# Performance work log

Measured on AMD Instinct MI355X. Metric: run time of the kernel, lower is better.

## Reference

```python
import jax, jax.numpy as jnp
import numpy as np

B, N, DE, DH, L, DC = 8, 256, 768, 192, 2, 192
NEG = 1e30  # mask_logic constant from the repo


def setup_inputs() -> dict:
    ks = iter(jax.random.split(jax.random.key(0), 32))

    def nrm(shape, s=0.02):
        return jax.random.normal(next(ks), shape, dtype=jnp.float32) * s

    features = jax.random.normal(next(ks), (B, N, DE), dtype=jnp.float32)
    # DAG adjacency: node i attends to a subset of j < i; guarantee edge (i, i-1)
    rnd = jax.random.bernoulli(next(ks), 0.3, (B, N, N))
    tril = jnp.tril(jnp.ones((N, N), jnp.bool_), -1)
    adj = ((rnd & tril[None]) | jnp.eye(N, k=-1, dtype=jnp.bool_)[None]).astype(jnp.float32)
    s_mask = jax.random.bernoulli(next(ks), 0.5, (B, N, N)).astype(jnp.float32)
    s_mask_onehot = jnp.stack([1.0 - s_mask, s_mask], axis=-1)  # unused in forward
    lengths = jnp.full((B,), N, dtype=jnp.int32)  # unused (nodal_att_type=None)
    return dict(
        features=features, adj=adj, s_mask=s_mask,
        s_mask_onehot=s_mask_onehot, lengths=lengths,
        fc1_w=nrm((DE, DH)), fc1_b=jnp.zeros((DH,), jnp.float32),
        gat_w=nrm((L, 2 * DH)), gat_b=jnp.zeros((L,), jnp.float32),
        wr0=nrm((L, DH, DH)), wr1=nrm((L, DH, DH)),
        gruc_wih=nrm((L, 3 * DH, DH)), gruc_whh=nrm((L, 3 * DH, DH)),
        gruc_bih=jnp.zeros((L, 3 * DH), jnp.float32),
        gruc_bhh=jnp.zeros((L, 3 * DH), jnp.float32),
        grup_wih=nrm((L, 3 * DH, DH)), grup_whh=nrm((L, 3 * DH, DH)),
        grup_bih=jnp.zeros((L, 3 * DH), jnp.float32),
        grup_bhh=jnp.zeros((L, 3 * DH), jnp.float32),
        mlp_w0=nrm((DH * (L + 1), DH)), mlp_b0=jnp.zeros((DH,), jnp.float32),
        mlp_w1=nrm((DH, DH)), mlp_b1=jnp.zeros((DH,), jnp.float32),
        mlp_w2=nrm((DH, DC)), mlp_b2=jnp.zeros((DC,), jnp.float32),
    )


def _gru(x, h, wih, whh, bih, bhh):
    # torch.nn.GRUCell math
    gi = x @ wih.T + bih
    gh = h @ whh.T + bhh
    ir, iz, inn = jnp.split(gi, 3, axis=-1)
    hr, hz, hn = jnp.split(gh, 3, axis=-1)
    r = jax.nn.sigmoid(ir + hr)
    z = jax.nn.sigmoid(iz + hz)
    n = jnp.tanh(inn + r * hn)
    return (1.0 - z) * n + z * h


def _layer(Hl, adj, s_mask, gat_w, gat_b, wr0, wr1, cw, cp):
    # One DAG layer: sequential scan over nodes. Carry holds the relation-
    # projected value buffers V0=H1@Wr0^T, V1=H1@Wr1^T and per-node key
    # scores Ksc=H1@wk (rows >= i are zero and masked out), which is
    # mathematically identical to the torch code that re-projects the
    # growing H1 every step.
    wq, wk = gat_w[:DH], gat_w[DH:]
    pos = jnp.arange(N)

    def step(carry, xs):
        V0, V1, Ksc = carry
        i, x_i, adj_i, sm_i = xs  # x_i:(B,DH) adj_i,sm_i:(B,N)
        score = (x_i @ wq)[:, None] + Ksc + gat_b          # (B,N)
        mask = (pos < i)[None, :] & (adj_i > 0.5)          # ragged :i slice
        alpha = jnp.where(mask, score, score - NEG)        # mask_logic
        attn = jax.nn.softmax(alpha, axis=-1)              # masked -> exactly 0
        Vrel = V0 * sm_i[..., None] + V1 * (1.0 - sm_i[..., None])
        M = jnp.einsum('bn,bnd->bd', attn, Vrel)
        M = jnp.where(i > 0, M, 0.0)                       # node 0: no context
        C = _gru(x_i, M, *cw)
        P = _gru(M, x_i, *cp)
        Hnew = C + P
        V0 = V0.at[:, i, :].set(Hnew @ wr0.T)
        V1 = V1.at[:, i, :].set(Hnew @ wr1.T)
        Ksc = Ksc.at[:, i].set(Hnew @ wk)
        attn_out = jnp.where(i > 0, attn, 0.0)             # adjB row 0 is zeros
        return (V0, V1, Ksc), (Hnew, attn_out)

    z3 = jnp.zeros((B, N, DH), jnp.float32)
    carry0 = (z3, z3, jnp.zeros((B, N), jnp.float32))
    xs = (pos, Hl.transpose(1, 0, 2), adj.transpose(1, 0, 2), s_mask.transpose(1, 0, 2))
    _, (Hseq, Aseq) = jax.lax.scan(step, carry0, xs)
    return Hseq.transpose(1, 0, 2), Aseq.transpose(1, 0, 2)  # (B,N,DH),(B,N,N)


def reference(features, adj, s_mask, s_mask_onehot, lengths,
              fc1_w, fc1_b, gat_w, gat_b, wr0, wr1,
              gruc_wih, gruc_whh, gruc_bih, gruc_bhh,
              grup_wih, grup_whh, grup_bih, grup_bhh,
              mlp_w0, mlp_b0, mlp_w1, mlp_b1, mlp_w2, mlp_b2):
    Hl = jax.nn.relu(features @ fc1_w + fc1_b)  # H0
    Hs, As = [Hl], []
    for l in range(L):
        cw = (gruc_wih[l], gruc_whh[l], gruc_bih[l], gruc_bhh[l])
        cp = (grup_wih[l], grup_whh[l], grup_bih[l], grup_bhh[l])
        Hl, Al = _layer(Hl, adj, s_mask, gat_w[l], gat_b[l], wr0[l], wr1[l], cw, cp)
        Hs.append(Hl)
        As.append(Al)
    H = jnp.concatenate(Hs, axis=2)  # (B,N,DH*(L+1))
    # nodal_att_type=None => attentive_node_features is identity
    h = jax.nn.relu(H @ mlp_w0 + mlp_b0)
    h = jax.nn.relu(h @ mlp_w1 + mlp_b1)  # mlp_layers-1 = 1 extra block
    logits = h @ mlp_w2 + mlp_b2          # dropout: eval-mode identity
    return logits, jnp.stack(As, axis=1)  # (B,N,DC), (B,L,N,N)
```

## Files before the change

kernel.cpp:

```cpp
#include <hip/hip_runtime.h>
#include <stdint.h>

#define B_  8
#define N_  256
#define DH_ 192
#define L_  2
#define G3  576
#define G6  1152
#define NW  4
#define DS  48
#define KD  24
#define GC  288
#define STH 10001
#define STP 20001
#define STQ 25001
#define SPK 50000
#define SF1 50001
#define SF2 50002
#define SDN 60001

typedef unsigned long long u64;

__device__ __forceinline__ float bflo(uint32_t u) { return __uint_as_float(u << 16); }
__device__ __forceinline__ float bfhi(uint32_t u) { return __uint_as_float(u & 0xffff0000u); }
__device__ __forceinline__ uint32_t f2bf(float f) {
    uint32_t x = __float_as_uint(f);
    x += 0x7fffu + ((x >> 16) & 1u);
    return x >> 16;
}
__device__ __forceinline__ float sigm(float x)  { return 1.f / (1.f + __expf(-x)); }
__device__ __forceinline__ float tanhf_(float x){ return 1.f - 2.f / (1.f + __expf(2.f * x)); }
__device__ __forceinline__ u64 packvs(float v, int st) {
    return ((u64)(uint32_t)st << 32) | __float_as_uint(v);
}
__device__ __forceinline__ u64 agload(const u64* p) {
    return __hip_atomic_load(p, __ATOMIC_RELAXED, __HIP_MEMORY_SCOPE_AGENT);
}
__device__ __forceinline__ void agstore(u64* p, u64 v) {
    __hip_atomic_store(p, v, __ATOMIC_RELAXED, __HIP_MEMORY_SCOPE_AGENT);
}

struct ScanSm {
    uint4 Wr4s[12 * DH_];
    float sA0[2][N_], sA1[2][N_], sKsc[N_];
    float sAdjN[N_], sSmN[N_];
    float sXq[DH_], sPre[6 * DS], sXv[DS];
    float sM[DH_], su0[DS], su1[DS], sGc[GC], sHn[DS];
    float sRedS[2][4], sRedX[3], sSaved[4];
};
struct WorkSm {
    float sX[DH_];
    float sPv[GC];
    float sRed[3];
};
struct PrologSm {
    float sA[8][768];
    float sRed[3][8][192];
};
struct MlpSm {
    float sH[8][576];
    float sRed[3][8][192];
    float sT[8][192];
};
union SmemAll { ScanSm s; WorkSm w; PrologSm p; MlpSm m; };

__device__ void prepack_slice(int idx,
    const float* __restrict__ wr0, const float* __restrict__ wr1,
    const float* __restrict__ c_wih, const float* __restrict__ c_whh,
    const float* __restrict__ c_bih, const float* __restrict__ c_bhh,
    const float* __restrict__ p_wih, const float* __restrict__ p_whh,
    const float* __restrict__ p_bih, const float* __restrict__ p_bhh,
    float* __restrict__ WpreT, uint32_t* __restrict__ W4,
    uint32_t* __restrict__ Wr4, uint32_t* __restrict__ Wp4w,
    float* __restrict__ biasPre, float* __restrict__ gbx)
{
    for (int l = 0; l < L_; ++l) {
        const float* cwih = c_wih + l * G3 * DH_;
        const float* cwhh = c_whh + l * G3 * DH_;
        const float* pwih = p_wih + l * G3 * DH_;
        const float* pwhh = p_whh + l * G3 * DH_;
        if (l == 0) {
            int k = idx / G6, r = idx - k * G6;
            float w = (r < G3) ? cwih[r * DH_ + k] : pwhh[(r - G3) * DH_ + k];
            WpreT[k * G6 + r] = w;
        }
        if (idx < NW * 27648) {
            int w = idx / 27648, pos = idx % 27648;
            int p4 = pos / 1152, rem = pos % 1152;
            int c2 = rem >> 2, s = rem & 3;
            int p = 4 * p4 + s;
            int j = c2 / DS, dd = c2 % DS;
            int c = 192 * j + DS * w + dd;
            float w0 = (c < G3) ? cwhh[c * DH_ + 2 * p]     : pwih[(c - G3) * DH_ + 2 * p];
            float w1 = (c < G3) ? cwhh[c * DH_ + 2 * p + 1] : pwih[(c - G3) * DH_ + 2 * p + 1];
            W4[l * NW * 27648 + idx] = f2bf(w0) | (f2bf(w1) << 16);
            if (l == 1) {
                int r = c;
                float v0 = (r < G3) ? cwih[r * DH_ + 2 * p]     : pwhh[(r - G3) * DH_ + 2 * p];
                float v1 = (r < G3) ? cwih[r * DH_ + 2 * p + 1] : pwhh[(r - G3) * DH_ + 2 * p + 1];
                Wp4w[idx] = f2bf(v0) | (f2bf(v1) << 16);
            }
        }
        if (idx < NW * 9216) {
            int w = idx / 9216, pos = idx % 9216;
            int kq = pos / 768, rem = pos % 768;
            int d = rem >> 2, s = rem & 3;
            int k = DS * w + 4 * kq + s;
            Wr4[l * NW * 9216 + idx] =
                f2bf(wr0[l * DH_ * DH_ + d * DH_ + k]) |
                (f2bf(wr1[l * DH_ * DH_ + d * DH_ + k]) << 16);
        }
        if (idx < G6) {
            float base = (idx < G3) ? c_bih[l * G3 + idx] : p_bhh[l * G3 + idx - G3];
            float fold = 0.f;
            if (idx < 384)                    fold = c_bhh[l * G3 + idx];
            else if (idx >= G3 && idx < 960)  fold = p_bih[l * G3 + idx - G3];
            biasPre[l * G6 + idx] = base + fold;
        }
        if (idx < 384) {
            gbx[l * 384 + idx] = (idx < DH_) ? c_bhh[l * G3 + 384 + idx]
                                             : p_bih[l * G3 + 384 + (idx - DH_)];
        }
    }
}

__device__ void flag_sync(u64* flags, int wgid, int t, int stamp)
{
    __threadfence();
    __syncthreads();
    if (t == 0) agstore(&flags[wgid], packvs(0.f, stamp));
    if (t < 96) {
        while ((uint32_t)(agload(&flags[t]) >> 32) != (uint32_t)stamp) {}
    }
    __syncthreads();
    __threadfence();
    __syncthreads();
}

__device__ void prologue(char* smem, int wgid, int t,
    const float* __restrict__ features, const float* __restrict__ fc1_w,
    const float* __restrict__ fc1_b, const float* __restrict__ WpreT,
    const float* __restrict__ biasPre,
    float* __restrict__ Hcat, float* __restrict__ PREg, u64* __restrict__ Fp)
{
    PrologSm* P = (PrologSm*)smem;
    const int c = t % 192, kg = t / 192;
    for (int tt = wgid; tt < 256; tt += 96) {
        const int r0 = tt * 8;
        for (int q = t; q < 1536; q += 576) {
            int r = q / 192, c4 = q % 192;
            *(float4*)&P->sA[r][4 * c4] = *(const float4*)(features + (size_t)(r0 + r) * 768 + 4 * c4);
        }
        __syncthreads();
        {
            const float* bp = fc1_w + (size_t)(kg * 256) * 192 + c;
            float acc[8] = {0.f, 0.f, 0.f, 0.f, 0.f, 0.f, 0.f, 0.f};
            #pragma unroll 8
            for (int kk = 0; kk < 256; ++kk) {
                float bv = bp[(size_t)kk * 192];
                #pragma unroll
                for (int rr = 0; rr < 8; ++rr) acc[rr] += P->sA[rr][kg * 256 + kk] * bv;
            }
            #pragma unroll
            for (int rr = 0; rr < 8; ++rr) P->sRed[kg][rr][c] = acc[rr];
        }
        __syncthreads();
        if (t < 192) {
            float bv = fc1_b[t];
            #pragma unroll
            for (int rr = 0; rr < 8; ++rr) {
                float v = P->sRed[0][rr][t] + P->sRed[1][rr][t] + P->sRed[2][rr][t] + bv;
                Hcat[(size_t)(r0 + rr) * G3 + t] = fmaxf(v, 0.f);
            }
        }
        __syncthreads();
    }
    flag_sync(Fp + 96, wgid, t, SF1);
    {
        const float bpa = biasPre[t], bpb = biasPre[576 + t];
        for (int tt = wgid; tt < 256; tt += 96) {
            const int r0 = tt * 8;
            for (int q = t; q < 384; q += 576) {
                int r = q / 48, c4 = q % 48;
                *(float4*)&P->sA[r][4 * c4] = *(const float4*)(Hcat + (size_t)(r0 + r) * G3 + 4 * c4);
            }
            __syncthreads();
            {
                const float* b0 = WpreT + t;
                float a0[8] = {0.f,0.f,0.f,0.f,0.f,0.f,0.f,0.f};
                float a1[8] = {0.f,0.f,0.f,0.f,0.f,0.f,0.f,0.f};
                #pragma unroll 4
                for (int k = 0; k < 192; ++k) {
                    float bva = b0[(size_t)k * G6];
                    float bvb = b0[(size_t)k * G6 + 576];
                    #pragma unroll
                    for (int rr = 0; rr < 8; ++rr) {
                        float av = P->sA[rr][k];
                        a0[rr] += av * bva; a1[rr] += av * bvb;
                    }
                }
                #pragma unroll
                for (int rr = 0; rr < 8; ++rr) {
                    PREg[(size_t)(r0 + rr) * G6 + t]       = a0[rr] + bpa;
                    PREg[(size_t)(r0 + rr) * G6 + 576 + t] = a1[rr] + bpb;
                }
            }
            __syncthreads();
        }
    }
    flag_sync(Fp + 192, wgid, t, SF2);
}

__device__ void mlp_tail(char* smem, int wgid, int t,
    const float* __restrict__ Hcat,
    const float* __restrict__ mw0, const float* __restrict__ mb0,
    const float* __restrict__ mw1, const float* __restrict__ mb1,
    const float* __restrict__ mw2, const float* __restrict__ mb2,
    float* __restrict__ out, u64* __restrict__ Fd)
{
    if (t < 64) {
        while ((uint32_t)(agload(&Fd[t]) >> 32) != (uint32_t)SDN) {}
    }
    __syncthreads();
    __threadfence();
    __syncthreads();
    MlpSm* M = (MlpSm*)smem;
    const int c = t % 192, kg = t / 192;
    for (int tt = wgid; tt < 256; tt += 96) {
        const int r0 = tt * 8;
        for (int q = t; q < 1152; q += 576) {
            int r = q / 144, c4 = q % 144;
            *(float4*)&M->sH[r][4 * c4] = *(const float4*)(Hcat + (size_t)(r0 + r) * G3 + 4 * c4);
        }
        __syncthreads();
        {
            const float* bp = mw0 + (size_t)(kg * 192) * 192 + c;
            float acc[8] = {0.f,0.f,0.f,0.f,0.f,0.f,0.f,0.f};
            #pragma unroll 8
            for (int kk = 0; kk < 192; ++kk) {
                float bv = bp[(size_t)kk * 192];
                #pragma unroll
                for (int rr = 0; rr < 8; ++rr) acc[rr] += M->sH[rr][kg * 192 + kk] * bv;
            }
            #pragma unroll
            for (int rr = 0; rr < 8; ++rr) M->sRed[kg][rr][c] = acc[rr];
        }
        __syncthreads();
        if (t < 192) {
            float bv = mb0[t];
            #pragma unroll
            for (int rr = 0; rr < 8; ++rr)
                M->sT[rr][t] = fmaxf(M->sRed[0][rr][t] + M->sRed[1][rr][t] + M->sRed[2][rr][t] + bv, 0.f);
        }
        __syncthreads();
        {
            const float* bp = mw1 + (size_t)(kg * 64) * 192 + c;
            float acc[8] = {0.f,0.f,0.f,0.f,0.f,0.f,0.f,0.f};
            #pragma unroll 8
            for (int kk = 0; kk < 64; ++kk) {
                float bv = bp[(size_t)kk * 192];
                #pragma unroll
                for (int rr = 0; rr < 8; ++rr) acc[rr] += M->sT[rr][kg * 64 + kk] * bv;
            }
            #pragma unroll
            for (int rr = 0; rr < 8; ++rr) M->sRed[kg][rr][c] = acc[rr];
        }
        __syncthreads();
        if (t < 192) {
            float bv = mb1[t];
            #pragma unroll
            for (int rr = 0; rr < 8; ++rr)
                M->sH[rr][t] = fmaxf(M->sRed[0][rr][t] + M->sRed[1][rr][t] + M->sRed[2][rr][t] + bv, 0.f);
        }
        __syncthreads();
        {
            const float* bp = mw2 + (size_t)(kg * 64) * 192 + c;
            float acc[8] = {0.f,0.f,0.f,0.f,0.f,0.f,0.f,0.f};
            #pragma unroll 8
            for (int kk = 0; kk < 64; ++kk) {
                float bv = bp[(size_t)kk * 192];
                #pragma unroll
                for (int rr = 0; rr < 8; ++rr) acc[rr] += M->sH[rr][kg * 64 + kk] * bv;
            }
            #pragma unroll
            for (int rr = 0; rr < 8; ++rr) M->sRed[kg][rr][c] = acc[rr];
        }
        __syncthreads();
        if (t < 192) {
            float bv = mb2[t];
            #pragma unroll
            for (int rr = 0; rr < 8; ++rr)
                out[(size_t)(r0 + rr) * 192 + t] =
                    M->sRed[0][rr][t] + M->sRed[1][rr][t] + M->sRed[2][rr][t] + bv;
        }
        __syncthreads();
    }
}

template<int ISL2>
__device__ void scan_body(
    ScanSm* S, int b, int w, int t,
    const float* __restrict__ xin, float* __restrict__ hout,
    const float* __restrict__ PREg, const float* __restrict__ adj,
    const float* __restrict__ smask,
    const uint32_t* __restrict__ W4l, const uint32_t* __restrict__ Wr4l,
    const float* __restrict__ gbxl, const float* __restrict__ gatwl,
    uint32_t* __restrict__ Hw, u64* __restrict__ MPsl, u64* __restrict__ Kdl,
    u64* __restrict__ HcW, const u64* __restrict__ HcR,
    const u64* __restrict__ PREcR, const u64* __restrict__ XQcR,
    float* __restrict__ AsB, int sbase)
{
    const int lane = t & 63, wave = t >> 6;
    const int dg0 = w * DS;
    const float* adjB = adj   + (size_t)b * N_ * N_;
    const float* smB  = smask + (size_t)b * N_ * N_;
    const int fi = b * NW;
    const int cB4 = t >> 1, khB4 = t & 1;

    {
        uint32_t* wr = (uint32_t*)S->Wr4s;
        for (int q = t; q < 9216; q += 576) wr[q] = Wr4l[q];
    }
    uint4 wreg[12];
    {
        const uint4* W4v = (const uint4*)W4l;
        #pragma unroll
        for (int p4 = 0; p4 < 12; ++p4) wreg[p4] = W4v[(12 * khB4 + p4) * GC + cB4];
    }
    float wqv = (!ISL2 && t < DH_) ? gatwl[t] : 0.f;
    float wkv = 0.f, g2b = 0.f, g5b = 0.f;
    if (t < DS) { wkv = gatwl[DH_ + dg0 + t]; g2b = gbxl[dg0 + t]; g5b = gbxl[DH_ + dg0 + t]; }
    if (t < N_) { S->sKsc[t] = 0.f; S->sA0[1][t] = 0.f; S->sA1[1][t] = 0.f; }
    if (t < DS) { S->su0[t] = 0.f; S->su1[t] = 0.f; }
    if (t < 4)  S->sRedS[1][t] = 0.f;
    if (w == 0 && t < N_) AsB[t] = 0.f;

    if (!ISL2) {
        if (t < DS) {
            const float* pre = PREg + (size_t)(b * N_) * G6 + dg0 + t;
            S->sPre[t] = pre[0]; S->sPre[DS + t] = pre[192]; S->sPre[2 * DS + t] = pre[384];
            S->sPre[3 * DS + t] = pre[576]; S->sPre[4 * DS + t] = pre[768]; S->sPre[5 * DS + t] = pre[960];
            S->sXv[t] = xin[(size_t)(b * N_) * G3 + dg0 + t];
        }
        for (int q = t; q < 176; q += 576) {
            if (q < 64)       *(float4*)&S->sAdjN[4 * q] = *(const float4*)(adjB + N_ + 4 * q);
            else if (q < 128) { int q2 = q - 64;  *(float4*)&S->sSmN[4 * q2] = *(const float4*)(smB + N_ + 4 * q2); }
            else              { int q2 = q - 128; *(float4*)&S->sXq[4 * q2] = *(const float4*)(xin + (size_t)(b * N_ + 1) * G3 + 4 * q2); }
        }
    } else {
        for (int q = t; q < 321; q += 576) {
            if (q < 64)       *(float4*)&S->sAdjN[4 * q] = *(const float4*)(adjB + N_ + 4 * q);
            else if (q < 128) { int q2 = q - 64;  *(float4*)&S->sSmN[4 * q2] = *(const float4*)(smB + N_ + 4 * q2); }
            else if (q < 176) {
                int d = q - 128;
                const u64* p = HcR + ((size_t)(b * N_) * NW + w) * DS + d;
                u64 v; do { v = agload(p); } while ((uint32_t)(v >> 32) != (uint32_t)STH);
                S->sXv[d] = __uint_as_float((uint32_t)v);
            } else if (q < 320) {
                int qq = q - 176;
                const u64* p = PREcR + ((size_t)(b * N_) * NW + w) * 144 + qq;
                u64 v; do { v = agload(p); } while ((uint32_t)(v >> 32) != (uint32_t)STP);
                uint32_t pl = (uint32_t)v;
                S->sPre[2 * qq] = bflo(pl); S->sPre[2 * qq + 1] = bfhi(pl);
            } else {
                const u64* p = XQcR + b * N_ + 1;
                u64 v; do { v = agload(p); } while ((uint32_t)(v >> 32) != (uint32_t)(STQ + 1));
                S->sSaved[3] = __uint_as_float((uint32_t)v);
            }
        }
    }
    __syncthreads();
    {
        float hn = 0.f;
        if (t < DS) {
            float xv = S->sXv[t];
            float r1 = sigm(S->sPre[t]), z1 = sigm(S->sPre[DS + t]);
            float n1 = tanhf_(S->sPre[2 * DS + t] + r1 * g2b);
            float Cv = (1.f - z1) * n1;
            float r2 = sigm(S->sPre[3 * DS + t]), z2 = sigm(S->sPre[4 * DS + t]);
            float n2 = tanhf_(g5b + r2 * S->sPre[5 * DS + t]);
            hn = Cv + (1.f - z2) * n2 + z2 * xv;
            S->sHn[t] = hn;
            hout[(size_t)(b * N_) * G3 + dg0 + t] = hn;
            if (!ISL2) HcW[((size_t)(b * N_) * NW + w) * DS + t] = packvs(hn, STH);
        }
        if (t == 0) { S->sSaved[0] = S->sAdjN[0]; S->sSaved[1] = S->sSmN[0]; }
        if (wave == 0) {
            float v = hn * wkv;
            #pragma unroll
            for (int o = 32; o; o >>= 1) v += __shfl_xor(v, o);
            if (lane == 0) agstore(&Kdl[fi + w], packvs(v, sbase));
        }
    }
    __syncthreads();
    if (t < KD) Hw[(size_t)t * N_] = f2bf(S->sHn[2 * t]) | (f2bf(S->sHn[2 * t + 1]) << 16);
    if (!ISL2) {
        float px = (t < DH_) ? S->sXq[t] * wqv : 0.f;
        #pragma unroll
        for (int o = 32; o; o >>= 1) px += __shfl_xor(px, o);
        if (t < DH_ && lane == 0) S->sRedX[wave] = px;
    }
    __syncthreads();
    float xqc = ISL2 ? S->sSaved[3] : (S->sRedX[0] + S->sRedX[1] + S->sRedX[2]);

    for (int i = 1; i < N_; ++i) {
        const int row = b * N_ + i;
        const int stamp = sbase + i;
        const int pp = i & 1, pn = pp ^ 1;

        if (t >= 384) {
            const int u = t - 384;
            const int inx = (i + 1 < N_) ? i + 1 : N_ - 1;
            if (!ISL2) {
                for (int qq = u; qq < 260; qq += 192) {
                    if (qq < 64)
                        *(float4*)&S->sAdjN[4 * qq] = *(const float4*)(adjB + (size_t)inx * N_ + 4 * qq);
                    else if (qq < 128) { int q2 = qq - 64;
                        *(float4*)&S->sSmN[4 * q2] = *(const float4*)(smB + (size_t)inx * N_ + 4 * q2); }
                    else if (qq < 140) { int q2 = qq - 128;
                        *(float4*)&S->sXv[4 * q2] = *(const float4*)(xin + (size_t)row * G3 + dg0 + 4 * q2); }
                    else if (qq < 212) { int q2 = qq - 140; int g = q2 / 12, o = q2 - 12 * g;
                        *(float4*)&S->sPre[g * DS + 4 * o] =
                            *(const float4*)(PREg + (size_t)row * G6 + g * DH_ + dg0 + 4 * o); }
                    else { int q2 = qq - 212;
                        *(float4*)&S->sXq[4 * q2] = *(const float4*)(xin + (size_t)(b * N_ + inx) * G3 + 4 * q2); }
                }
            } else {
                for (int qq = u; qq < 321; qq += 192) {
                    if (qq < 64)
                        *(float4*)&S->sAdjN[4 * qq] = *(const float4*)(adjB + (size_t)inx * N_ + 4 * qq);
                    else if (qq < 128) { int q2 = qq - 64;
                        *(float4*)&S->sSmN[4 * q2] = *(const float4*)(smB + (size_t)inx * N_ + 4 * q2); }
                    else if (qq < 176) {
                        int d = qq - 128;
                        const u64* p = HcR + ((size_t)row * NW + w) * DS + d;
                        u64 v; do { v = agload(p); } while ((uint32_t)(v >> 32) != (uint32_t)(STH + i));
                        S->sXv[d] = __uint_as_float((uint32_t)v);
                    } else if (qq < 320) {
                        int q2 = qq - 176;
                        const u64* p = PREcR + ((size_t)row * NW + w) * 144 + q2;
                        u64 v; do { v = agload(p); } while ((uint32_t)(v >> 32) != (uint32_t)(STP + i));
                        uint32_t pl = (uint32_t)v;
                        S->sPre[2 * q2] = bflo(pl); S->sPre[2 * q2 + 1] = bfhi(pl);
                    } else {
                        const u64* p = XQcR + b * N_ + inx;
                        u64 v; do { v = agload(p); } while ((uint32_t)(v >> 32) != (uint32_t)(STQ + inx));
                        S->sSaved[3] = __uint_as_float((uint32_t)v);
                    }
                }
            }
            if (t == 575) {
                const uint32_t ex = (uint32_t)(stamp - 1);
                u64 k0, k1, k2, k3;
                do {
                    k0 = agload(&Kdl[fi + 0]); k1 = agload(&Kdl[fi + 1]);
                    k2 = agload(&Kdl[fi + 2]); k3 = agload(&Kdl[fi + 3]);
                } while ((uint32_t)(k0 >> 32) != ex || (uint32_t)(k1 >> 32) != ex ||
                         (uint32_t)(k2 >> 32) != ex || (uint32_t)(k3 >> 32) != ex);
                float kdot = __uint_as_float((uint32_t)k0) + __uint_as_float((uint32_t)k1)
                           + __uint_as_float((uint32_t)k2) + __uint_as_float((uint32_t)k3);
                float adjI1 = S->sSaved[0], smI1 = S->sSaved[1];
                float e1 = (adjI1 > 0.5f) ? __expf(xqc + kdot) : 0.f;
                float Ssum = S->sRedS[pp][0] + S->sRedS[pp][1] + S->sRedS[pp][2] + S->sRedS[pp][3] + e1;
                S->sKsc[i - 1] = kdot;
                float c0 = e1 * smI1;
                S->sA0[pp][i - 1] = c0; S->sA1[pp][i - 1] = e1 - c0;
                S->sSaved[2] = 1.f / Ssum;
            }
        }
        __syncthreads();

        if (t < DH_) {
            float mp = 0.f, h0a = 0.f, h1a = 0.f;
            #pragma unroll 4
            for (int kq = 0; kq < 12; ++kq) {
                uint4 wv = S->Wr4s[kq * DH_ + t];
                const int k0 = 4 * kq;
                float lo, hi;
                lo = bflo(wv.x); hi = bfhi(wv.x);
                mp = fmaf(S->su0[k0 + 0], lo, mp); mp = fmaf(S->su1[k0 + 0], hi, mp);
                h0a = fmaf(S->sHn[k0 + 0], lo, h0a); h1a = fmaf(S->sHn[k0 + 0], hi, h1a);
                lo = bflo(wv.y); hi = bfhi(wv.y);
                mp = fmaf(S->su0[k0 + 1], lo, mp); mp = fmaf(S->su1[k0 + 1], hi, mp);
                h0a = fmaf(S->sHn[k0 + 1], lo, h0a); h1a = fmaf(S->sHn[k0 + 1], hi, h1a);
                lo = bflo(wv.z); hi = bfhi(wv.z);
                mp = fmaf(S->su0[k0 + 2], lo, mp); mp = fmaf(S->su1[k0 + 2], hi, mp);
                h0a = fmaf(S->sHn[k0 + 2], lo, h0a); h1a = fmaf(S->sHn[k0 + 2], hi, h1a);
                lo = bflo(wv.w); hi = bfhi(wv.w);
                mp = fmaf(S->su0[k0 + 3], lo, mp); mp = fmaf(S->su1[k0 + 3], hi, mp);
                h0a = fmaf(S->sHn[k0 + 3], lo, h0a); h1a = fmaf(S->sHn[k0 + 3], hi, h1a);
            }
            float invS = S->sSaved[2];
            mp = (mp + S->sA0[pp][i - 1] * h0a + S->sA1[pp][i - 1] * h1a) * invS;
            S->sM[t] = mp;
            agstore(&MPsl[(size_t)(fi + w) * DH_ + t], packvs(mp, stamp));
            if (!ISL2) {
                float px = S->sXq[t] * wqv;
                #pragma unroll
                for (int o = 32; o; o >>= 1) px += __shfl_xor(px, o);
                if (lane == 0) S->sRedX[wave] = px;
            }
        } else if (w == 0 && t < 448) {
            int j = t - 192;
            AsB[(size_t)i * N_ + j] = (S->sA0[pp][j] + S->sA1[pp][j]) * S->sSaved[2];
        }
        __syncthreads();

        const float xqn = ISL2 ? S->sSaved[3] : (S->sRedX[0] + S->sRedX[1] + S->sRedX[2]);
        if (t < N_) {
            float e = 0.f;
            if (t == i) { S->sSaved[0] = S->sAdjN[t]; S->sSaved[1] = S->sSmN[t]; }
            if (t < i && S->sAdjN[t] > 0.5f) e = __expf(xqn + S->sKsc[t]);
            float b0 = e * S->sSmN[t];
            S->sA0[pn][t] = b0; S->sA1[pn][t] = e - b0;
            float ps = e;
            #pragma unroll
            for (int o = 32; o; o >>= 1) ps += __shfl_xor(ps, o);
            if (lane == 0) S->sRedS[pn][wave] = ps;
        }
        __syncthreads();

        if (t < 384) {
            const int ilim = i;
            const int kd = t >> 4, jp = t & 15;
            const uint32_t* hp = Hw + (size_t)kd * N_;
            float u0l = 0.f, u0h = 0.f, u1l = 0.f, u1h = 0.f;
            int j = jp;
            while (j + 48 < ilim) {
                uint32_t h0 = hp[j], h1 = hp[j + 16], h2 = hp[j + 32], h3 = hp[j + 48];
                float b0, b1;
                b0 = S->sA0[pn][j];      b1 = S->sA1[pn][j];
                u0l = fmaf(b0, bflo(h0), u0l); u0h = fmaf(b0, bfhi(h0), u0h);
                u1l = fmaf(b1, bflo(h0), u1l); u1h = fmaf(b1, bfhi(h0), u1h);
                b0 = S->sA0[pn][j + 16]; b1 = S->sA1[pn][j + 16];
                u0l = fmaf(b0, bflo(h1), u0l); u0h = fmaf(b0, bfhi(h1), u0h);
                u1l = fmaf(b1, bflo(h1), u1l); u1h = fmaf(b1, bfhi(h1), u1h);
                b0 = S->sA0[pn][j + 32]; b1 = S->sA1[pn][j + 32];
                u0l = fmaf(b0, bflo(h2), u0l); u0h = fmaf(b0, bfhi(h2), u0h);
                u1l = fmaf(b1, bflo(h2), u1l); u1h = fmaf(b1, bfhi(h2), u1h);
                b0 = S->sA0[pn][j + 48]; b1 = S->sA1[pn][j + 48];
                u0l = fmaf(b0, bflo(h3), u0l); u0h = fmaf(b0, bfhi(h3), u0h);
                u1l = fmaf(b1, bflo(h3), u1l); u1h = fmaf(b1, bfhi(h3), u1h);
                j += 64;
            }
            for (; j < ilim; j += 16) {
                uint32_t hv = hp[j];
                float b0 = S->sA0[pn][j], b1 = S->sA1[pn][j];
                u0l = fmaf(b0, bflo(hv), u0l); u0h = fmaf(b0, bfhi(hv), u0h);
                u1l = fmaf(b1, bflo(hv), u1l); u1h = fmaf(b1, bfhi(hv), u1h);
            }
            #pragma unroll
            for (int o = 1; o <= 8; o <<= 1) {
                u0l += __shfl_xor(u0l, o); u0h += __shfl_xor(u0h, o);
                u1l += __shfl_xor(u1l, o); u1h += __shfl_xor(u1h, o);
            }
            if (jp == 0) {
                S->su0[2 * kd] = u0l; S->su0[2 * kd + 1] = u0h;
                S->su1[2 * kd] = u1l; S->su1[2 * kd + 1] = u1h;
            }
        } else {
            const int d = t - 384;
            const int w1 = (w + 1) & 3, w2 = (w + 2) & 3, w3 = (w + 3) & 3;
            u64* pA = &MPsl[(size_t)(fi + w1) * DH_ + d];
            u64* pB = &MPsl[(size_t)(fi + w2) * DH_ + d];
            u64* pC = &MPsl[(size_t)(fi + w3) * DH_ + d];
            const uint32_t ex = (uint32_t)stamp;
            u64 vA, vB, vC;
            do {
                vA = agload(pA); vB = agload(pB); vC = agload(pC);
            } while ((uint32_t)(vA >> 32) != ex || (uint32_t)(vB >> 32) != ex ||
                     (uint32_t)(vC >> 32) != ex);
            S->sM[d] += __uint_as_float((uint32_t)vA)
                      + __uint_as_float((uint32_t)vB)
                      + __uint_as_float((uint32_t)vC);
        }
        __syncthreads();

        {
            float g = 0.f;
            #pragma unroll
            for (int p4 = 0; p4 < 12; ++p4) {
                const uint4 wv = wreg[p4];
                const int m0 = 8 * (12 * khB4 + p4);
                g = fmaf(S->sM[m0 + 0], bflo(wv.x), g); g = fmaf(S->sM[m0 + 1], bfhi(wv.x), g);
                g = fmaf(S->sM[m0 + 2], bflo(wv.y), g); g = fmaf(S->sM[m0 + 3], bfhi(wv.y), g);
                g = fmaf(S->sM[m0 + 4], bflo(wv.z), g); g = fmaf(S->sM[m0 + 5], bfhi(wv.z), g);
                g = fmaf(S->sM[m0 + 6], bflo(wv.w), g); g = fmaf(S->sM[m0 + 7], bfhi(wv.w), g);
            }
            g += __shfl_xor(g, 1);
            if (khB4 == 0) S->sGc[cB4] = g;
        }
        __syncthreads();

        {
            float hn = 0.f;
            if (t < DS) {
                float Mv = S->sM[dg0 + t];
                float r1 = sigm(S->sPre[t] + S->sGc[t]);
                float z1 = sigm(S->sPre[DS + t] + S->sGc[DS + t]);
                float n1 = tanhf_(S->sPre[2 * DS + t] + r1 * (S->sGc[2 * DS + t] + g2b));
                float Cv = (1.f - z1) * n1 + z1 * Mv;
                float r2 = sigm(S->sGc[3 * DS + t] + S->sPre[3 * DS + t]);
                float z2 = sigm(S->sGc[4 * DS + t] + S->sPre[4 * DS + t]);
                float n2 = tanhf_(S->sGc[5 * DS + t] + g5b + r2 * S->sPre[5 * DS + t]);
                hn = Cv + (1.f - z2) * n2 + z2 * S->sXv[t];
                S->sHn[t] = hn;
                hout[(size_t)row * G3 + dg0 + t] = hn;
                if (!ISL2) HcW[((size_t)row * NW + w) * DS + t] = packvs(hn, STH + i);
            }
            if (wave == 0) {
                float v = hn * wkv;
                #pragma unroll
                for (int o = 32; o; o >>= 1) v += __shfl_xor(v, o);
                if (lane == 0) agstore(&Kdl[fi + w], packvs(v, stamp));
            }
            if (t < KD) Hw[(size_t)t * N_ + i] = f2bf(S->sHn[2 * t]) | (f2bf(S->sHn[2 * t + 1]) << 16);
        }
        __syncthreads();
        xqc = xqn;
    }
}

__device__ void worker_body(WorkSm* Wm, int b, int w, int t,
    const uint32_t* __restrict__ Wp4g, const float* __restrict__ bias2,
    const float* __restrict__ wq2,
    const u64* __restrict__ HcR, u64* __restrict__ PREcW, u64* __restrict__ XQcW)
{
    const int lane = t & 63, wave = t >> 6;
    const int c = t >> 1, kh = t & 1;
    uint4 wpreg[12];
    {
        const uint4* v4 = (const uint4*)Wp4g;
        #pragma unroll
        for (int p4 = 0; p4 < 12; ++p4) wpreg[p4] = v4[(12 * kh + p4) * GC + c];
    }
    float bv = 0.f;
    if (kh == 0) bv = bias2[192 * (c / DS) + w * DS + (c % DS)];
    float wqt = (t < DH_) ? wq2[t] : 0.f;
    for (int i = 0; i < N_; ++i) {
        if (t < DH_) {
            const u64* p = HcR + ((size_t)(b * N_ + i) * NW + (t / DS)) * DS + (t % DS);
            u64 v; do { v = agload(p); } while ((uint32_t)(v >> 32) != (uint32_t)(STH + i));
            Wm->sX[t] = __uint_as_float((uint32_t)v);
        }
        __syncthreads();
        {
            float g = 0.f;
            #pragma unroll
            for (int p4 = 0; p4 < 12; ++p4) {
                const uint4 wv = wpreg[p4];
                const int m0 = 8 * (12 * kh + p4);
                g = fmaf(Wm->sX[m0 + 0], bflo(wv.x), g); g = fmaf(Wm->sX[m0 + 1], bfhi(wv.x), g);
                g = fmaf(Wm->sX[m0 + 2], bflo(wv.y), g); g = fmaf(Wm->sX[m0 + 3], bfhi(wv.y), g);
                g = fmaf(Wm->sX[m0 + 4], bflo(wv.z), g); g = fmaf(Wm->sX[m0 + 5], bfhi(wv.z), g);
                g = fmaf(Wm->sX[m0 + 6], bflo(wv.w), g); g = fmaf(Wm->sX[m0 + 7], bfhi(wv.w), g);
            }
            g += __shfl_xor(g, 1);
            if (kh == 0) Wm->sPv[c] = g + bv;
        }
        if (w == 0) {
            float px = (t < DH_) ? Wm->sX[t] * wqt : 0.f;
            #pragma unroll
            for (int o = 32; o; o >>= 1) px += __shfl_xor(px, o);
            if (t < DH_ && lane == 0) Wm->sRed[wave] = px;
        }
        __syncthreads();
        if (t < 144) {
            u64 v = ((u64)(uint32_t)(STP + i) << 32)
                  | f2bf(Wm->sPv[2 * t]) | (f2bf(Wm->sPv[2 * t + 1]) << 16);
            agstore(&PREcW[((size_t)(b * N_ + i) * NW + w) * 144 + t], v);
        }
        if (w == 0 && t == 0)
            agstore(&XQcW[b * N_ + i],
                    packvs(Wm->sRed[0] + Wm->sRed[1] + Wm->sRed[2], STQ + i));
        __syncthreads();
    }
}

__global__ __launch_bounds__(576, 1) void pipeline_kernel(
    const float* __restrict__ features, const float* __restrict__ fc1_w,
    const float* __restrict__ fc1_b,
    const float* __restrict__ adj, const float* __restrict__ smask,
    const float* __restrict__ gatw,
    const float* __restrict__ wr0, const float* __restrict__ wr1,
    const float* __restrict__ c_wih, const float* __restrict__ c_whh,
    const float* __restrict__ c_bih, const float* __restrict__ c_bhh,
    const float* __restrict__ p_wih, const float* __restrict__ p_whh,
    const float* __restrict__ p_bih, const float* __restrict__ p_bhh,
    const float* __restrict__ mw0, const float* __restrict__ mb0,
    const float* __restrict__ mw1, const float* __restrict__ mb1,
    const float* __restrict__ mw2, const float* __restrict__ mb2,
    float* __restrict__ Hcat, float* __restrict__ PREg,
    float* __restrict__ WpreT, uint32_t* __restrict__ W4,
    uint32_t* __restrict__ Wr4, uint32_t* __restrict__ Wp4w,
    float* __restrict__ biasPre, float* __restrict__ gbx,
    uint32_t* __restrict__ Hb, u64* __restrict__ MPs, u64* __restrict__ Kd,
    u64* __restrict__ Hc, u64* __restrict__ PREc, u64* __restrict__ XQc,
    u64* __restrict__ Fp, u64* __restrict__ Fd,
    float* __restrict__ out)
{
    __shared__ __align__(16) char smem[sizeof(SmemAll)];
    const int blk = blockIdx.x, t = threadIdx.x;
    const int wgid = blk;
    const int b = blk & 7, r12 = blk >> 3;
    const int role = r12 >> 2, w = r12 & 3;

    for (int j = 0; j < 4; ++j) {
        int idx = wgid * 576 + t + 55296 * j;
        prepack_slice(idx, wr0, wr1, c_wih, c_whh, c_bih, c_bhh,
                      p_wih, p_whh, p_bih, p_bhh,
                      WpreT, W4, Wr4, Wp4w, biasPre, gbx);
    }
    flag_sync(Fp, wgid, t, SPK);

    prologue(smem, wgid, t, features, fc1_w, fc1_b, WpreT, biasPre,
             Hcat, PREg, Fp);

    float* As = out + 393216;
    if (role == 0) {
        scan_body<0>((ScanSm*)smem, b, w, t,
            Hcat, Hcat + 192, PREg, adj, smask,
            W4, Wr4, gbx, gatw,
            Hb + (size_t)(b * NW + w) * KD * N_, MPs, Kd,
            Hc, nullptr, nullptr, nullptr,
            As + (size_t)b * (L_ * N_ * N_), 1);
        __threadfence();
        __syncthreads();
        if (t == 0) agstore(&Fd[b * 8 + w], packvs(0.f, SDN));
    } else if (role == 2) {
        scan_body<1>((ScanSm*)smem, b, w, t,
            nullptr, Hcat + 384, nullptr, adj, smask,
            W4 + NW * 27648, Wr4 + NW * 9216, gbx + 384, gatw + 384,
            Hb + (size_t)(32 + b * NW + w) * KD * N_,
            MPs + (size_t)8 * NW * DH_, Kd + 8 * NW,
            nullptr, Hc, PREc, XQc,
            As + (size_t)b * (L_ * N_ * N_) + N_ * N_, 30001);
        __threadfence();
        __syncthreads();
        if (t == 0) agstore(&Fd[b * 8 + 4 + w], packvs(0.f, SDN));
    } else {
        worker_body((WorkSm*)smem, b, w, t,
            Wp4w + (size_t)w * 27648, biasPre + G6, gatw + 384,
            Hc, PREc, XQc);
    }

    mlp_tail(smem, wgid, t, Hcat, mw0, mb0, mw1, mb1, mw2, mb2, out, Fd);
}

extern "C" void kernel_launch(void* const* d_in, const int* in_sizes, int n_in,
                              void* d_out, int out_size, void* d_ws, size_t ws_size,
                              hipStream_t stream)
{
    const float* features = (const float*)d_in[0];
    const float* adj      = (const float*)d_in[1];
    const float* smask    = (const float*)d_in[2];
    const float* fc1_w = (const float*)d_in[5];
    const float* fc1_b = (const float*)d_in[6];
    const float* gat_w = (const float*)d_in[7];
    const float* wr0   = (const float*)d_in[9];
    const float* wr1   = (const float*)d_in[10];
    const float* c_wih = (const float*)d_in[11];
    const float* c_whh = (const float*)d_in[12];
    const float* c_bih = (const float*)d_in[13];
    const float* c_bhh = (const float*)d_in[14];
    const float* p_wih = (const float*)d_in[15];
    const float* p_whh = (const float*)d_in[16];
    const float* p_bih = (const float*)d_in[17];
    const float* p_bhh = (const float*)d_in[18];
    const float* mw0 = (const float*)d_in[19];
    const float* mb0 = (const float*)d_in[20];
    const float* mw1 = (const float*)d_in[21];
    const float* mb1 = (const float*)d_in[22];
    const float* mw2 = (const float*)d_in[23];
    const float* mb2 = (const float*)d_in[24];
    float* out = (float*)d_out;

    char* wsb = (char*)d_ws;
    size_t off = 0;
    auto carve = [&](size_t bytes) -> char* {
        char* p = wsb + off;
        off = (off + bytes + 255) & ~(size_t)255;
        return p;
    };
    float* Hcat     = (float*)carve(2048ull * 576 * 4);
    float* PREg     = (float*)carve(2048ull * 1152 * 4);
    float* WpreT    = (float*)carve(192ull * 1152 * 4);
    uint32_t* W4    = (uint32_t*)carve(2ull * NW * 27648 * 4);
    uint32_t* Wr4   = (uint32_t*)carve(2ull * NW * 9216 * 4);
    uint32_t* Wp4w  = (uint32_t*)carve((size_t)NW * 27648 * 4);
    float* biasPre  = (float*)carve(2ull * 1152 * 4);
    float* gbx      = (float*)carve(2ull * 384 * 4);
    uint32_t* Hb    = (uint32_t*)carve(64ull * KD * 256 * 4);
    u64* MPs        = (u64*)carve(2ull * 8 * NW * DH_ * 8);
    u64* Kd         = (u64*)carve(2ull * 8 * NW * 8);
    u64* Hc         = (u64*)carve(8ull * 256 * NW * DS * 8);
    u64* PREc       = (u64*)carve(8ull * 256 * NW * 144 * 8);
    u64* XQc        = (u64*)carve(8ull * 256 * 8);
    u64* Fp         = (u64*)carve(288ull * 8);
    u64* Fd         = (u64*)carve(64ull * 8);

    pipeline_kernel<<<dim3(96), 576, 0, stream>>>(
        features, fc1_w, fc1_b, adj, smask, gat_w,
        wr0, wr1, c_wih, c_whh, c_bih, c_bhh, p_wih, p_whh, p_bih, p_bhh,
        mw0, mb0, mw1, mb1, mw2, mb2,
        Hcat, PREg, WpreT, W4, Wr4, Wp4w, biasPre, gbx,
        Hb, MPs, Kd, Hc, PREc, XQc, Fp, Fd, out);
}
```

Before: 1.932 ms.

## Fold relation projections into GRU weights and exchange per-slice state instead of full messages

Precomputes fused weights WfG = (GRU recurrent/input weights) x (Wr0/Wr1), so the scan's gate GEMV consumes the per-slice attention sums directly instead of a separately projected message. The cross-workgroup exchange changes from publishing the full 192-wide projected message plus key dots to publishing each slice's new hidden values, partial attention sums and key dot in one stamped buffer. Each workgroup gathers its siblings' slices and recomputes the message locally. The change doubles the per-thread weight registers and adds a prologue GEMM, in exchange for cutting one serialized matvec and barrier from the per-node critical path.

Result: slower. 3.936 ms (+103.7%).

```diff
diff --git a/kernel.cpp b/kernel.cpp
--- a/kernel.cpp
+++ b/kernel.cpp
@@ -11,6 +11,8 @@
 #define DS  48
 #define KD  24
 #define GC  288
+#define HSW 160
+#define HSR (2 * 8 * NW * HSW)
 #define STH 10001
 #define STP 20001
 #define STQ 25001
@@ -39,14 +41,20 @@
 __device__ __forceinline__ void agstore(u64* p, u64 v) {
     __hip_atomic_store(p, v, __ATOMIC_RELAXED, __HIP_MEMORY_SCOPE_AGENT);
 }
+__device__ __forceinline__ float u2f(u64 v) { return __uint_as_float((uint32_t)v); }
 
 struct ScanSm {
-    uint4 Wr4s[12 * DH_];
-    float sA0[2][N_], sA1[2][N_], sKsc[N_];
+    uint32_t wrS[192 * 49];
+    float sV0[DH_], sV1[DH_];
+    float sHnF[DH_], sSu0f[DH_], sSu1f[DH_];
+    float sA0[N_], sA1[N_];
+    float sKsc[N_];
     float sAdjN[N_], sSmN[N_];
-    float sXq[DH_], sPre[6 * DS], sXv[DS];
-    float sM[DH_], su0[DS], su1[DS], sGc[GC], sHn[DS];
-    float sRedS[2][4], sRedX[3], sSaved[4];
+    float sXq[2][DH_];
+    float sPre[6 * DS], sXv[DS];
+    float sGc[GC], sMv[DS], sHn[DS];
+    float su0[DS], su1[DS];
+    float sRedS[8], sRedX[4], sKdP[4], sSaved[8], sSavedA[2], sSavedS[2];
 };
 struct WorkSm {
     float sX[DH_];
@@ -70,42 +78,33 @@
     const float* __restrict__ c_bih, const float* __restrict__ c_bhh,
     const float* __restrict__ p_wih, const float* __restrict__ p_whh,
     const float* __restrict__ p_bih, const float* __restrict__ p_bhh,
-    float* __restrict__ WpreT, uint32_t* __restrict__ W4,
-    uint32_t* __restrict__ Wr4, uint32_t* __restrict__ Wp4w,
+    float* __restrict__ WpreT, uint32_t* __restrict__ Wr4,
+    uint32_t* __restrict__ Wp4w,
     float* __restrict__ biasPre, float* __restrict__ gbx)
 {
     for (int l = 0; l < L_; ++l) {
         const float* cwih = c_wih + l * G3 * DH_;
-        const float* cwhh = c_whh + l * G3 * DH_;
-        const float* pwih = p_wih + l * G3 * DH_;
         const float* pwhh = p_whh + l * G3 * DH_;
         if (l == 0) {
             int k = idx / G6, r = idx - k * G6;
             float w = (r < G3) ? cwih[r * DH_ + k] : pwhh[(r - G3) * DH_ + k];
             WpreT[k * G6 + r] = w;
         }
-        if (idx < NW * 27648) {
+        if (l == 1 && idx < NW * 27648) {
             int w = idx / 27648, pos = idx % 27648;
             int p4 = pos / 1152, rem = pos % 1152;
             int c2 = rem >> 2, s = rem & 3;
             int p = 4 * p4 + s;
             int j = c2 / DS, dd = c2 % DS;
-            int c = 192 * j + DS * w + dd;
-            float w0 = (c < G3) ? cwhh[c * DH_ + 2 * p]     : pwih[(c - G3) * DH_ + 2 * p];
-            float w1 = (c < G3) ? cwhh[c * DH_ + 2 * p + 1] : pwih[(c - G3) * DH_ + 2 * p + 1];
-            W4[l * NW * 27648 + idx] = f2bf(w0) | (f2bf(w1) << 16);
-            if (l == 1) {
-                int r = c;
-                float v0 = (r < G3) ? cwih[r * DH_ + 2 * p]     : pwhh[(r - G3) * DH_ + 2 * p];
-                float v1 = (r < G3) ? cwih[r * DH_ + 2 * p + 1] : pwhh[(r - G3) * DH_ + 2 * p + 1];
-                Wp4w[idx] = f2bf(v0) | (f2bf(v1) << 16);
-            }
+            int r = 192 * j + DS * w + dd;
+            float v0 = (r < G3) ? cwih[r * DH_ + 2 * p]     : pwhh[(r - G3) * DH_ + 2 * p];
+            float v1 = (r < G3) ? cwih[r * DH_ + 2 * p + 1] : pwhh[(r - G3) * DH_ + 2 * p + 1];
+            Wp4w[idx] = f2bf(v0) | (f2bf(v1) << 16);
         }
         if (idx < NW * 9216) {
             int w = idx / 9216, pos = idx % 9216;
-            int kq = pos / 768, rem = pos % 768;
-            int d = rem >> 2, s = rem & 3;
-            int k = DS * w + 4 * kq + s;
+            int k = pos / 48, dl = pos % 48;
+            int d = w * DS + dl;
             Wr4[l * NW * 9216 + idx] =
                 f2bf(wr0[l * DH_ * DH_ + d * DH_ + k]) |
                 (f2bf(wr1[l * DH_ * DH_ + d * DH_ + k]) << 16);
@@ -122,6 +121,36 @@
                                              : p_bih[l * G3 + 384 + (idx - DH_)];
         }
     }
+}
+
+__device__ void wf_tile(int wgid, int t,
+    const float* __restrict__ wr0, const float* __restrict__ wr1,
+    const float* __restrict__ c_whh, const float* __restrict__ p_wih,
+    uint32_t* __restrict__ WfG)
+{
+    const int jj = t / 12, kblk = t % 12;
+    const int job = wgid * 48 + jj;
+    const int l = job / 2304, r = job % 2304;
+    const int mat = r / 1152, cg = r % 1152;
+    const float* wcp = (cg < G3) ? (c_whh + (size_t)(l * G3 + cg) * DH_)
+                                 : (p_wih + (size_t)(l * G3 + cg - G3) * DH_);
+    const float* wrp = (mat == 0 ? wr0 : wr1) + (size_t)l * DH_ * DH_;
+    const int k0 = kblk * 16;
+    float acc[16];
+    #pragma unroll
+    for (int z = 0; z < 16; ++z) acc[z] = 0.f;
+    for (int d = 0; d < DH_; ++d) {
+        const float wc = wcp[d];
+        const float* wrd = wrp + (size_t)d * DH_ + k0;
+        #pragma unroll
+        for (int z = 0; z < 16; ++z) acc[z] = fmaf(wc, wrd[z], acc[z]);
+    }
+    const int wdst = (cg % 192) / 48;
+    const int c2 = (cg / 192) * 48 + (cg % 48);
+    uint32_t* dst = WfG + (((size_t)l * NW + wdst) * 288 + c2) * 192 + mat * 96 + (k0 >> 1);
+    #pragma unroll
+    for (int z = 0; z < 8; ++z)
+        dst[z] = f2bf(acc[2 * z]) | (f2bf(acc[2 * z + 1]) << 16);
 }
 
 __device__ void flag_sync(u64* flags, int wgid, int t, int stamp)
@@ -303,9 +332,9 @@
     const float* __restrict__ xin, float* __restrict__ hout,
     const float* __restrict__ PREg, const float* __restrict__ adj,
     const float* __restrict__ smask,
-    const uint32_t* __restrict__ W4l, const uint32_t* __restrict__ Wr4l,
+    const uint32_t* __restrict__ WfGl, const uint32_t* __restrict__ Wr4l,
     const float* __restrict__ gbxl, const float* __restrict__ gatwl,
-    uint32_t* __restrict__ Hw, u64* __restrict__ MPsl, u64* __restrict__ Kdl,
+    uint32_t* __restrict__ Hw, u64* __restrict__ HSrole,
     u64* __restrict__ HcW, const u64* __restrict__ HcR,
     const u64* __restrict__ PREcR, const u64* __restrict__ XQcR,
     float* __restrict__ AsB, int sbase)
@@ -314,26 +343,33 @@
     const int dg0 = w * DS;
     const float* adjB = adj   + (size_t)b * N_ * N_;
     const float* smB  = smask + (size_t)b * N_ * N_;
-    const int fi = b * NW;
     const int cB4 = t >> 1, khB4 = t & 1;
 
     {
-        uint32_t* wr = (uint32_t*)S->Wr4s;
-        for (int q = t; q < 9216; q += 576) wr[q] = Wr4l[q];
-    }
-    uint4 wreg[12];
+        const uint32_t* wrG = Wr4l + (size_t)w * 9216;
+        for (int q = t; q < 9216; q += 576) {
+            int k = q / 48, dl = q - 48 * k;
+            S->wrS[k * 49 + dl] = wrG[q];
+        }
+    }
+    uint4 wfreg[24];
     {
-        const uint4* W4v = (const uint4*)W4l;
+        const uint4* wfb = (const uint4*)(WfGl + ((size_t)w * 288 + cB4) * 192);
         #pragma unroll
-        for (int p4 = 0; p4 < 12; ++p4) wreg[p4] = W4v[(12 * khB4 + p4) * GC + cB4];
-    }
-    float wqv = (!ISL2 && t < DH_) ? gatwl[t] : 0.f;
+        for (int p4 = 0; p4 < 12; ++p4) {
+            wfreg[p4]      = wfb[khB4 * 12 + p4];
+            wfreg[12 + p4] = wfb[24 + khB4 * 12 + p4];
+        }
+    }
+    float wqx = (!ISL2 && t >= 192 && t < 384) ? gatwl[t - 192] : 0.f;
     float wkv = 0.f, g2b = 0.f, g5b = 0.f;
     if (t < DS) { wkv = gatwl[DH_ + dg0 + t]; g2b = gbxl[dg0 + t]; g5b = gbxl[DH_ + dg0 + t]; }
-    if (t < N_) { S->sKsc[t] = 0.f; S->sA0[1][t] = 0.f; S->sA1[1][t] = 0.f; }
+    if (t < N_) { S->sKsc[t] = 0.f; S->sA0[t] = 0.f; S->sA1[t] = 0.f; }
     if (t < DS) { S->su0[t] = 0.f; S->su1[t] = 0.f; }
-    if (t < 4)  S->sRedS[1][t] = 0.f;
+    if (t < 8)  S->sRedS[t] = 0.f;
     if (w == 0 && t < N_) AsB[t] = 0.f;
+
+    u64* myHS0 = HSrole + ((size_t)b * NW + w) * HSW;
 
     if (!ISL2) {
         if (t < DS) {
@@ -342,10 +378,11 @@
             S->sPre[3 * DS + t] = pre[576]; S->sPre[4 * DS + t] = pre[768]; S->sPre[5 * DS + t] = pre[960];
             S->sXv[t] = xin[(size_t)(b * N_) * G3 + dg0 + t];
         }
-        for (int q = t; q < 176; q += 576) {
+        for (int q = t; q < 224; q += 576) {
             if (q < 64)       *(float4*)&S->sAdjN[4 * q] = *(const float4*)(adjB + N_ + 4 * q);
             else if (q < 128) { int q2 = q - 64;  *(float4*)&S->sSmN[4 * q2] = *(const float4*)(smB + N_ + 4 * q2); }
-            else              { int q2 = q - 128; *(float4*)&S->sXq[4 * q2] = *(const float4*)(xin + (size_t)(b * N_ + 1) * G3 + 4 * q2); }
+            else if (q < 176) { int q2 = q - 128; *(float4*)&S->sXq[1][4 * q2] = *(const float4*)(xin + (size_t)(b * N_ + 1) * G3 + 4 * q2); }
+            else              { int q2 = q - 176; *(float4*)&S->sXq[0][4 * q2] = *(const float4*)(xin + (size_t)(b * N_ + 2) * G3 + 4 * q2); }
         }
     } else {
         for (int q = t; q < 321; q += 576) {
@@ -383,22 +420,24 @@
             S->sHn[t] = hn;
             hout[(size_t)(b * N_) * G3 + dg0 + t] = hn;
             if (!ISL2) HcW[((size_t)(b * N_) * NW + w) * DS + t] = packvs(hn, STH);
-        }
-        if (t == 0) { S->sSaved[0] = S->sAdjN[0]; S->sSaved[1] = S->sSmN[0]; }
+            agstore(myHS0 + t, packvs(hn, sbase));
+        }
+        if (t == 0) { S->sSavedA[0] = S->sAdjN[0]; S->sSavedS[0] = S->sSmN[0]; }
+        if (t < 96) agstore(myHS0 + 48 + t, packvs(0.f, sbase));
         if (wave == 0) {
             float v = hn * wkv;
             #pragma unroll
             for (int o = 32; o; o >>= 1) v += __shfl_xor(v, o);
-            if (lane == 0) agstore(&Kdl[fi + w], packvs(v, sbase));
+            if (lane == 0) { S->sSaved[6] = v; agstore(myHS0 + 144, packvs(v, sbase)); }
         }
     }
     __syncthreads();
     if (t < KD) Hw[(size_t)t * N_] = f2bf(S->sHn[2 * t]) | (f2bf(S->sHn[2 * t + 1]) << 16);
-    if (!ISL2) {
-        float px = (t < DH_) ? S->sXq[t] * wqv : 0.f;
+    if (!ISL2 && t >= 192 && t < 384) {
+        float px = S->sXq[1][t - 192] * wqx;
         #pragma unroll
         for (int o = 32; o; o >>= 1) px += __shfl_xor(px, o);
-        if (t < DH_ && lane == 0) S->sRedX[wave] = px;
+        if (lane == 0) S->sRedX[wave - 3] = px;
     }
     __syncthreads();
     float xqc = ISL2 ? S->sSaved[3] : (S->sRedX[0] + S->sRedX[1] + S->sRedX[2]);
@@ -406,13 +445,26 @@
     for (int i = 1; i < N_; ++i) {
         const int row = b * N_ + i;
         const int stamp = sbase + i;
-        const int pp = i & 1, pn = pp ^ 1;
-
-        if (t >= 384) {
-            const int u = t - 384;
+        const int mpar = (i - 1) & 1, sp = i & 1;
+        u64* myHS = HSrole + ((size_t)(sp * 8 + b) * NW + w) * HSW;
+
+        if (t < 435) {
+            const int sib = t / 145, idx = t - sib * 145;
+            const int wsrc = (w + 1 + sib) & 3;
+            const u64* p = HSrole + ((size_t)(mpar * 8 + b) * NW + wsrc) * HSW + idx;
+            const uint32_t ex = (uint32_t)(stamp - 1);
+            u64 v; do { v = agload(p); } while ((uint32_t)(v >> 32) != ex);
+            float f = u2f(v);
+            if (idx < 48)       S->sHnF[wsrc * DS + idx]        = f;
+            else if (idx < 96)  S->sSu0f[wsrc * DS + idx - 48]  = f;
+            else if (idx < 144) S->sSu1f[wsrc * DS + idx - 96]  = f;
+            else                S->sKdP[sib] = f;
+        } else {
+            const int u = t - 435;
             const int inx = (i + 1 < N_) ? i + 1 : N_ - 1;
             if (!ISL2) {
-                for (int qq = u; qq < 260; qq += 192) {
+                const int ixq = (i + 2 < N_) ? i + 2 : N_ - 1;
+                for (int qq = u; qq < 260; qq += 141) {
                     if (qq < 64)
                         *(float4*)&S->sAdjN[4 * qq] = *(const float4*)(adjB + (size_t)inx * N_ + 4 * qq);
                     else if (qq < 128) { int q2 = qq - 64;
@@ -423,10 +475,10 @@
                         *(float4*)&S->sPre[g * DS + 4 * o] =
                             *(const float4*)(PREg + (size_t)row * G6 + g * DH_ + dg0 + 4 * o); }
                     else { int q2 = qq - 212;
-                        *(float4*)&S->sXq[4 * q2] = *(const float4*)(xin + (size_t)(b * N_ + inx) * G3 + 4 * q2); }
+                        *(float4*)&S->sXq[i & 1][4 * q2] = *(const float4*)(xin + (size_t)(b * N_ + ixq) * G3 + 4 * q2); }
                 }
             } else {
-                for (int qq = u; qq < 321; qq += 192) {
+                for (int qq = u; qq < 321; qq += 141) {
                     if (qq < 64)
                         *(float4*)&S->sAdjN[4 * qq] = *(const float4*)(adjB + (size_t)inx * N_ + 4 * qq);
                     else if (qq < 128) { int q2 = qq - 64;
@@ -443,159 +495,95 @@
                         uint32_t pl = (uint32_t)v;
                         S->sPre[2 * q2] = bflo(pl); S->sPre[2 * q2 + 1] = bfhi(pl);
                     } else {
-                        const u64* p = XQcR + b * N_ + inx;
-                        u64 v; do { v = agload(p); } while ((uint32_t)(v >> 32) != (uint32_t)(STQ + inx));
+                        const int inq = (i + 1 < N_) ? i + 1 : N_ - 1;
+                        const u64* p = XQcR + b * N_ + inq;
+                        u64 v; do { v = agload(p); } while ((uint32_t)(v >> 32) != (uint32_t)(STQ + inq));
                         S->sSaved[3] = __uint_as_float((uint32_t)v);
                     }
                 }
             }
-            if (t == 575) {
-                const uint32_t ex = (uint32_t)(stamp - 1);
-                u64 k0, k1, k2, k3;
-                do {
-                    k0 = agload(&Kdl[fi + 0]); k1 = agload(&Kdl[fi + 1]);
-                    k2 = agload(&Kdl[fi + 2]); k3 = agload(&Kdl[fi + 3]);
-                } while ((uint32_t)(k0 >> 32) != ex || (uint32_t)(k1 >> 32) != ex ||
-                         (uint32_t)(k2 >> 32) != ex || (uint32_t)(k3 >> 32) != ex);
-                float kdot = __uint_as_float((uint32_t)k0) + __uint_as_float((uint32_t)k1)
-                           + __uint_as_float((uint32_t)k2) + __uint_as_float((uint32_t)k3);
-                float adjI1 = S->sSaved[0], smI1 = S->sSaved[1];
-                float e1 = (adjI1 > 0.5f) ? __expf(xqc + kdot) : 0.f;
-                float Ssum = S->sRedS[pp][0] + S->sRedS[pp][1] + S->sRedS[pp][2] + S->sRedS[pp][3] + e1;
-                S->sKsc[i - 1] = kdot;
-                float c0 = e1 * smI1;
-                S->sA0[pp][i - 1] = c0; S->sA1[pp][i - 1] = e1 - c0;
-                S->sSaved[2] = 1.f / Ssum;
-            }
-        }
-        __syncthreads();
-
-        if (t < DH_) {
-            float mp = 0.f, h0a = 0.f, h1a = 0.f;
-            #pragma unroll 4
-            for (int kq = 0; kq < 12; ++kq) {
-                uint4 wv = S->Wr4s[kq * DH_ + t];
-                const int k0 = 4 * kq;
-                float lo, hi;
-                lo = bflo(wv.x); hi = bfhi(wv.x);
-                mp = fmaf(S->su0[k0 + 0], lo, mp); mp = fmaf(S->su1[k0 + 0], hi, mp);
-                h0a = fmaf(S->sHn[k0 + 0], lo, h0a); h1a = fmaf(S->sHn[k0 + 0], hi, h1a);
-                lo = bflo(wv.y); hi = bfhi(wv.y);
-                mp = fmaf(S->su0[k0 + 1], lo, mp); mp = fmaf(S->su1[k0 + 1], hi, mp);
-                h0a = fmaf(S->sHn[k0 + 1], lo, h0a); h1a = fmaf(S->sHn[k0 + 1], hi, h1a);
-                lo = bflo(wv.z); hi = bfhi(wv.z);
-                mp = fmaf(S->su0[k0 + 2], lo, mp); mp = fmaf(S->su1[k0 + 2], hi, mp);
-                h0a = fmaf(S->sHn[k0 + 2], lo, h0a); h1a = fmaf(S->sHn[k0 + 2], hi, h1a);
-                lo = bflo(wv.w); hi = bfhi(wv.w);
-                mp = fmaf(S->su0[k0 + 3], lo, mp); mp = fmaf(S->su1[k0 + 3], hi, mp);
-                h0a = fmaf(S->sHn[k0 + 3], lo, h0a); h1a = fmaf(S->sHn[k0 + 3], hi, h1a);
-            }
-            float invS = S->sSaved[2];
-            mp = (mp + S->sA0[pp][i - 1] * h0a + S->sA1[pp][i - 1] * h1a) * invS;
-            S->sM[t] = mp;
-            agstore(&MPsl[(size_t)(fi + w) * DH_ + t], packvs(mp, stamp));
-            if (!ISL2) {
-                float px = S->sXq[t] * wqv;
+        }
+        __syncthreads();
+
+        {
+            const float kdot = S->sKdP[0] + S->sKdP[1] + S->sKdP[2] + S->sSaved[6];
+            const float e1 = (S->sSavedA[0] > 0.5f) ? __expf(xqc + kdot) : 0.f;
+            const float Ssum = S->sRedS[0] + S->sRedS[1] + S->sRedS[2] + S->sRedS[3] + e1;
+            const float invS = 1.f / Ssum;
+            const float e1c0 = e1 * S->sSavedS[0], e1c1 = e1 - e1c0;
+            if (t == 575) S->sKsc[i - 1] = kdot;
+            if (t < 192) {
+                const bool own = (t >= dg0) && (t < dg0 + DS);
+                const int tl = t - dg0;
+                const float hv = own ? S->sHn[tl] : S->sHnF[t];
+                const float s0 = own ? S->su0[tl] : S->sSu0f[t];
+                const float s1 = own ? S->su1[tl] : S->sSu1f[t];
+                S->sV0[t] = (s0 + e1c0 * hv) * invS;
+                S->sV1[t] = (s1 + e1c1 * hv) * invS;
+            } else if (!ISL2 && t < 384) {
+                float px = S->sXq[(i - 1) & 1][t - 192] * wqx;
                 #pragma unroll
                 for (int o = 32; o; o >>= 1) px += __shfl_xor(px, o);
-                if (lane == 0) S->sRedX[wave] = px;
-            }
-        } else if (w == 0 && t < 448) {
-            int j = t - 192;
-            AsB[(size_t)i * N_ + j] = (S->sA0[pp][j] + S->sA1[pp][j]) * S->sSaved[2];
-        }
-        __syncthreads();
-
-        const float xqn = ISL2 ? S->sSaved[3] : (S->sRedX[0] + S->sRedX[1] + S->sRedX[2]);
-        if (t < N_) {
-            float e = 0.f;
-            if (t == i) { S->sSaved[0] = S->sAdjN[t]; S->sSaved[1] = S->sSmN[t]; }
-            if (t < i && S->sAdjN[t] > 0.5f) e = __expf(xqn + S->sKsc[t]);
-            float b0 = e * S->sSmN[t];
-            S->sA0[pn][t] = b0; S->sA1[pn][t] = e - b0;
-            float ps = e;
-            #pragma unroll
-            for (int o = 32; o; o >>= 1) ps += __shfl_xor(ps, o);
-            if (lane == 0) S->sRedS[pn][wave] = ps;
-        }
-        __syncthreads();
-
-        if (t < 384) {
-            const int ilim = i;
-            const int kd = t >> 4, jp = t & 15;
-            const uint32_t* hp = Hw + (size_t)kd * N_;
-            float u0l = 0.f, u0h = 0.f, u1l = 0.f, u1h = 0.f;
-            int j = jp;
-            while (j + 48 < ilim) {
-                uint32_t h0 = hp[j], h1 = hp[j + 16], h2 = hp[j + 32], h3 = hp[j + 48];
-                float b0, b1;
-                b0 = S->sA0[pn][j];      b1 = S->sA1[pn][j];
-                u0l = fmaf(b0, bflo(h0), u0l); u0h = fmaf(b0, bfhi(h0), u0h);
-                u1l = fmaf(b1, bflo(h0), u1l); u1h = fmaf(b1, bfhi(h0), u1h);
-                b0 = S->sA0[pn][j + 16]; b1 = S->sA1[pn][j + 16];
-                u0l = fmaf(b0, bflo(h1), u0l); u0h = fmaf(b0, bfhi(h1), u0h);
-                u1l = fmaf(b1, bflo(h1), u1l); u1h = fmaf(b1, bfhi(h1), u1h);
-                b0 = S->sA0[pn][j + 32]; b1 = S->sA1[pn][j + 32];
-                u0l = fmaf(b0, bflo(h2), u0l); u0h = fmaf(b0, bfhi(h2), u0h);
-                u1l = fmaf(b1, bflo(h2), u1l); u1h = fmaf(b1, bfhi(h2), u1h);
-                b0 = S->sA0[pn][j + 48]; b1 = S->sA1[pn][j + 48];
-                u0l = fmaf(b0, bflo(h3), u0l); u0h = fmaf(b0, bfhi(h3), u0h);
-                u1l = fmaf(b1, bflo(h3), u1l); u1h = fmaf(b1, bfhi(h3), u1h);
-                j += 64;
-            }
-            for (; j < ilim; j += 16) {
-                uint32_t hv = hp[j];
-                float b0 = S->sA0[pn][j], b1 = S->sA1[pn][j];
-                u0l = fmaf(b0, bflo(hv), u0l); u0h = fmaf(b0, bfhi(hv), u0h);
-                u1l = fmaf(b1, bflo(hv), u1l); u1h = fmaf(b1, bfhi(hv), u1h);
-            }
-            #pragma unroll
-            for (int o = 1; o <= 8; o <<= 1) {
-                u0l += __shfl_xor(u0l, o); u0h += __shfl_xor(u0h, o);
-                u1l += __shfl_xor(u1l, o); u1h += __shfl_xor(u1h, o);
-            }
-            if (jp == 0) {
-                S->su0[2 * kd] = u0l; S->su0[2 * kd + 1] = u0h;
-                S->su1[2 * kd] = u1l; S->su1[2 * kd + 1] = u1h;
-            }
-        } else {
-            const int d = t - 384;
-            const int w1 = (w + 1) & 3, w2 = (w + 2) & 3, w3 = (w + 3) & 3;
-            u64* pA = &MPsl[(size_t)(fi + w1) * DH_ + d];
-            u64* pB = &MPsl[(size_t)(fi + w2) * DH_ + d];
-            u64* pC = &MPsl[(size_t)(fi + w3) * DH_ + d];
-            const uint32_t ex = (uint32_t)stamp;
-            u64 vA, vB, vC;
-            do {
-                vA = agload(pA); vB = agload(pB); vC = agload(pC);
-            } while ((uint32_t)(vA >> 32) != ex || (uint32_t)(vB >> 32) != ex ||
-                     (uint32_t)(vC >> 32) != ex);
-            S->sM[d] += __uint_as_float((uint32_t)vA)
-                      + __uint_as_float((uint32_t)vB)
-                      + __uint_as_float((uint32_t)vC);
+                if (lane == 0) S->sRedX[wave - 3] = px;
+            }
+            if (w == 0) {
+                if (t < 192) {
+                    if (t < i) AsB[(size_t)i * N_ + t] =
+                        (t < i - 1) ? (S->sA0[t] + S->sA1[t]) * invS : e1 * invS;
+                } else if (t >= 448 && t < 512) {
+                    const int jj = t - 256;
+                    if (jj < i) AsB[(size_t)i * N_ + jj] =
+                        (jj < i - 1) ? (S->sA0[jj] + S->sA1[jj]) * invS : e1 * invS;
+                }
+            }
         }
         __syncthreads();
 
         {
             float g = 0.f;
+            const int vb = 96 * khB4;
             #pragma unroll
             for (int p4 = 0; p4 < 12; ++p4) {
-                const uint4 wv = wreg[p4];
-                const int m0 = 8 * (12 * khB4 + p4);
-                g = fmaf(S->sM[m0 + 0], bflo(wv.x), g); g = fmaf(S->sM[m0 + 1], bfhi(wv.x), g);
-                g = fmaf(S->sM[m0 + 2], bflo(wv.y), g); g = fmaf(S->sM[m0 + 3], bfhi(wv.y), g);
-                g = fmaf(S->sM[m0 + 4], bflo(wv.z), g); g = fmaf(S->sM[m0 + 5], bfhi(wv.z), g);
-                g = fmaf(S->sM[m0 + 6], bflo(wv.w), g); g = fmaf(S->sM[m0 + 7], bfhi(wv.w), g);
+                const uint4 wv = wfreg[p4];
+                const float4 va = *(const float4*)&S->sV0[vb + 8 * p4];
+                const float4 vc = *(const float4*)&S->sV0[vb + 8 * p4 + 4];
+                g = fmaf(bflo(wv.x), va.x, g); g = fmaf(bfhi(wv.x), va.y, g);
+                g = fmaf(bflo(wv.y), va.z, g); g = fmaf(bfhi(wv.y), va.w, g);
+                g = fmaf(bflo(wv.z), vc.x, g); g = fmaf(bfhi(wv.z), vc.y, g);
+                g = fmaf(bflo(wv.w), vc.z, g); g = fmaf(bfhi(wv.w), vc.w, g);
+            }
+            #pragma unroll
+            for (int p4 = 0; p4 < 12; ++p4) {
+                const uint4 wv = wfreg[12 + p4];
+                const float4 va = *(const float4*)&S->sV1[vb + 8 * p4];
+                const float4 vc = *(const float4*)&S->sV1[vb + 8 * p4 + 4];
+                g = fmaf(bflo(wv.x), va.x, g); g = fmaf(bfhi(wv.x), va.y, g);
+                g = fmaf(bflo(wv.y), va.z, g); g = fmaf(bfhi(wv.y), va.w, g);
+                g = fmaf(bflo(wv.z), vc.x, g); g = fmaf(bfhi(wv.z), vc.y, g);
+                g = fmaf(bflo(wv.w), vc.z, g); g = fmaf(bfhi(wv.w), vc.w, g);
             }
             g += __shfl_xor(g, 1);
             if (khB4 == 0) S->sGc[cB4] = g;
+            if (t < 192) {
+                const int d = t >> 2, q = t & 3;
+                float m = 0.f;
+                #pragma unroll 8
+                for (int kk = 0; kk < 48; ++kk) {
+                    const int k = q * 48 + kk;
+                    const uint32_t wv = S->wrS[k * 49 + d];
+                    m = fmaf(bflo(wv), S->sV0[k], m);
+                    m = fmaf(bfhi(wv), S->sV1[k], m);
+                }
+                m += __shfl_xor(m, 1); m += __shfl_xor(m, 2);
+                if (q == 0) S->sMv[d] = m;
+            }
         }
         __syncthreads();
 
         {
             float hn = 0.f;
             if (t < DS) {
-                float Mv = S->sM[dg0 + t];
+                float Mv = S->sMv[t];
                 float r1 = sigm(S->sPre[t] + S->sGc[t]);
                 float z1 = sigm(S->sPre[DS + t] + S->sGc[DS + t]);
                 float n1 = tanhf_(S->sPre[2 * DS + t] + r1 * (S->sGc[2 * DS + t] + g2b));
@@ -607,14 +595,76 @@
                 S->sHn[t] = hn;
                 hout[(size_t)row * G3 + dg0 + t] = hn;
                 if (!ISL2) HcW[((size_t)row * NW + w) * DS + t] = packvs(hn, STH + i);
+                agstore(myHS + t, packvs(hn, stamp));
             }
             if (wave == 0) {
                 float v = hn * wkv;
                 #pragma unroll
                 for (int o = 32; o; o >>= 1) v += __shfl_xor(v, o);
-                if (lane == 0) agstore(&Kdl[fi + w], packvs(v, stamp));
-            }
-            if (t < KD) Hw[(size_t)t * N_ + i] = f2bf(S->sHn[2 * t]) | (f2bf(S->sHn[2 * t + 1]) << 16);
+                if (lane == 0) { S->sSaved[6] = v; agstore(myHS + 144, packvs(v, stamp)); }
+            }
+        }
+        __syncthreads();
+
+        const float xqn = ISL2 ? S->sSaved[3] : (S->sRedX[0] + S->sRedX[1] + S->sRedX[2]);
+        if (t < N_) {
+            if (t == i) { S->sSavedA[0] = S->sAdjN[t]; S->sSavedS[0] = S->sSmN[t]; }
+            float e = 0.f;
+            if (t < i && S->sAdjN[t] > 0.5f) e = __expf(xqn + S->sKsc[t]);
+            float b0v = e * S->sSmN[t];
+            S->sA0[t] = b0v; S->sA1[t] = e - b0v;
+            float ps = e;
+            #pragma unroll
+            for (int o = 32; o; o >>= 1) ps += __shfl_xor(ps, o);
+            if (lane == 0) S->sRedS[wave] = ps;
+        } else if (t < N_ + KD) {
+            const int kk2 = t - N_;
+            Hw[(size_t)kk2 * N_ + i] = f2bf(S->sHn[2 * kk2]) | (f2bf(S->sHn[2 * kk2 + 1]) << 16);
+        }
+        __syncthreads();
+
+        if (t < 384) {
+            const int ilim = i;
+            const int kd = t >> 4, jp = t & 15;
+            const uint32_t* hp = Hw + (size_t)kd * N_;
+            float u0l = 0.f, u0h = 0.f, u1l = 0.f, u1h = 0.f;
+            int j = jp;
+            while (j + 48 < ilim) {
+                uint32_t h0 = hp[j], h1 = hp[j + 16], h2 = hp[j + 32], h3 = hp[j + 48];
+                float b0, b1;
+                b0 = S->sA0[j];      b1 = S->sA1[j];
+                u0l = fmaf(b0, bflo(h0), u0l); u0h = fmaf(b0, bfhi(h0), u0h);
+                u1l = fmaf(b1, bflo(h0), u1l); u1h = fmaf(b1, bfhi(h0), u1h);
+                b0 = S->sA0[j + 16]; b1 = S->sA1[j + 16];
+                u0l = fmaf(b0, bflo(h1), u0l); u0h = fmaf(b0, bfhi(h1), u0h);
+                u1l = fmaf(b1, bflo(h1), u1l); u1h = fmaf(b1, bfhi(h1), u1h);
+                b0 = S->sA0[j + 32]; b1 = S->sA1[j + 32];
+                u0l = fmaf(b0, bflo(h2), u0l); u0h = fmaf(b0, bfhi(h2), u0h);
+                u1l = fmaf(b1, bflo(h2), u1l); u1h = fmaf(b1, bfhi(h2), u1h);
+                b0 = S->sA0[j + 48]; b1 = S->sA1[j + 48];
+                u0l = fmaf(b0, bflo(h3), u0l); u0h = fmaf(b0, bfhi(h3), u0h);
+                u1l = fmaf(b1, bflo(h3), u1l); u1h = fmaf(b1, bfhi(h3), u1h);
+                j += 64;
+            }
+            for (; j < ilim; j += 16) {
+                uint32_t hv = hp[j];
+                float b0 = S->sA0[j], b1 = S->sA1[j];
+                u0l = fmaf(b0, bflo(hv), u0l); u0h = fmaf(b0, bfhi(hv), u0h);
+                u1l = fmaf(b1, bflo(hv), u1l); u1h = fmaf(b1, bfhi(hv), u1h);
+            }
+            #pragma unroll
+            for (int o = 1; o <= 8; o <<= 1) {
+                u0l += __shfl_xor(u0l, o); u0h += __shfl_xor(u0h, o);
+                u1l += __shfl_xor(u1l, o); u1h += __shfl_xor(u1h, o);
+            }
+            if (jp == 0) {
+                S->su0[2 * kd] = u0l; S->su0[2 * kd + 1] = u0h;
+                S->su1[2 * kd] = u1l; S->su1[2 * kd + 1] = u1h;
+                agstore(myHS + 48 + 2 * kd,     packvs(u0l, stamp));
+                agstore(myHS + 48 + 2 * kd + 1, packvs(u0h, stamp));
+                agstore(myHS + 96 + 2 * kd,     packvs(u1l, stamp));
+                agstore(myHS + 96 + 2 * kd + 1, packvs(u1h, stamp));
+            }
         }
         __syncthreads();
         xqc = xqn;
@@ -691,10 +741,10 @@
     const float* __restrict__ mw1, const float* __restrict__ mb1,
     const float* __restrict__ mw2, const float* __restrict__ mb2,
     float* __restrict__ Hcat, float* __restrict__ PREg,
-    float* __restrict__ WpreT, uint32_t* __restrict__ W4,
+    float* __restrict__ WpreT, uint32_t* __restrict__ WfG,
     uint32_t* __restrict__ Wr4, uint32_t* __restrict__ Wp4w,
     float* __restrict__ biasPre, float* __restrict__ gbx,
-    uint32_t* __restrict__ Hb, u64* __restrict__ MPs, u64* __restrict__ Kd,
+    uint32_t* __restrict__ Hb, u64* __restrict__ HS,
     u64* __restrict__ Hc, u64* __restrict__ PREc, u64* __restrict__ XQc,
     u64* __restrict__ Fp, u64* __restrict__ Fd,
     float* __restrict__ out)
@@ -709,8 +759,9 @@
         int idx = wgid * 576 + t + 55296 * j;
         prepack_slice(idx, wr0, wr1, c_wih, c_whh, c_bih, c_bhh,
                       p_wih, p_whh, p_bih, p_bhh,
-                      WpreT, W4, Wr4, Wp4w, biasPre, gbx);
-    }
+                      WpreT, Wr4, Wp4w, biasPre, gbx);
+    }
+    wf_tile(wgid, t, wr0, wr1, c_whh, p_wih, WfG);
     flag_sync(Fp, wgid, t, SPK);
 
     prologue(smem, wgid, t, features, fc1_w, fc1_b, WpreT, biasPre,
@@ -720,8 +771,8 @@
     if (role == 0) {
         scan_body<0>((ScanSm*)smem, b, w, t,
             Hcat, Hcat + 192, PREg, adj, smask,
-            W4, Wr4, gbx, gatw,
-            Hb + (size_t)(b * NW + w) * KD * N_, MPs, Kd,
+            WfG, Wr4, gbx, gatw,
+            Hb + (size_t)(b * NW + w) * KD * N_, HS,
             Hc, nullptr, nullptr, nullptr,
             As + (size_t)b * (L_ * N_ * N_), 1);
         __threadfence();
@@ -730,9 +781,8 @@
     } else if (role == 2) {
         scan_body<1>((ScanSm*)smem, b, w, t,
             nullptr, Hcat + 384, nullptr, adj, smask,
-            W4 + NW * 27648, Wr4 + NW * 9216, gbx + 384, gatw + 384,
-            Hb + (size_t)(32 + b * NW + w) * KD * N_,
-            MPs + (size_t)8 * NW * DH_, Kd + 8 * NW,
+            WfG + (size_t)NW * 288 * 192, Wr4 + NW * 9216, gbx + 384, gatw + 384,
+            Hb + (size_t)(32 + b * NW + w) * KD * N_, HS + HSR,
             nullptr, Hc, PREc, XQc,
             As + (size_t)b * (L_ * N_ * N_) + N_ * N_, 30001);
         __threadfence();
@@ -785,14 +835,13 @@
     float* Hcat     = (float*)carve(2048ull * 576 * 4);
     float* PREg     = (float*)carve(2048ull * 1152 * 4);
     float* WpreT    = (float*)carve(192ull * 1152 * 4);
-    uint32_t* W4    = (uint32_t*)carve(2ull * NW * 27648 * 4);
+    uint32_t* WfG   = (uint32_t*)carve(2ull * NW * 288 * 192 * 4);
     uint32_t* Wr4   = (uint32_t*)carve(2ull * NW * 9216 * 4);
     uint32_t* Wp4w  = (uint32_t*)carve((size_t)NW * 27648 * 4);
     float* biasPre  = (float*)carve(2ull * 1152 * 4);
     float* gbx      = (float*)carve(2ull * 384 * 4);
     uint32_t* Hb    = (uint32_t*)carve(64ull * KD * 256 * 4);
-    u64* MPs        = (u64*)carve(2ull * 8 * NW * DH_ * 8);
-    u64* Kd         = (u64*)carve(2ull * 8 * NW * 8);
+    u64* HS         = (u64*)carve(2ull * HSR * 8);
     u64* Hc         = (u64*)carve(8ull * 256 * NW * DS * 8);
     u64* PREc       = (u64*)carve(8ull * 256 * NW * 144 * 8);
     u64* XQc        = (u64*)carve(8ull * 256 * 8);
@@ -803,6 +852,6 @@
         features, fc1_w, fc1_b, adj, smask, gat_w,
         wr0, wr1, c_wih, c_whh, c_bih, c_bhh, p_wih, p_whh, p_bih, p_bhh,
         mw0, mb0, mw1, mb1, mw2, mb2,
-        Hcat, PREg, WpreT, W4, Wr4, Wp4w, biasPre, gbx,
-        Hb, MPs, Kd, Hc, PREc, XQc, Fp, Fd, out);
-}
+        Hcat, PREg, WpreT, WfG, Wr4, Wp4w, biasPre, gbx,
+        Hb, HS, Hc, PREc, XQc, Fp, Fd, out);
+}
```
